# Kernel tuning notes

Hardware: AMD Instinct MI355X
Metric: run time of the kernel (lower is better)

The kernel has to match this reference:

```python
import jax, jax.numpy as jnp
import numpy as np

N, E, G = 50000, 800000, 64
IN, HID, T, EDGE_DIM, HLS = 32, 64, 2, 2, 32
# deg histogram: all nodes degree 16 -> avg_deg['log'] = log(16+1)
AVG_LOG = float(np.log(17.0))


def _pna(x, src, dst, eattr, We, be, Wpre, bpre, Wpost, bpost, Wlin, blin):
    """PNAConv with aggregators [mean,min,max,std], scalers [identity,amp,att],
    towers=T, pre_layers=1, post_layers=1, divide_input=False."""
    n, F = x.shape
    enc = eattr @ We + be                                   # [E, F] edge encoder
    # message: concat(x_i, x_j, edge) -> per-tower Linear(3F -> F)
    h = jnp.concatenate([x[dst], x[src], enc], axis=-1)     # [E, 3F] (same for all towers)
    m = jnp.einsum('ef,tfo->eto', h, Wpre) + bpre           # [E, T, F]
    ones = jnp.ones((m.shape[0],), m.dtype)
    cnt = jax.ops.segment_sum(ones, dst, num_segments=n)    # in-degree [N]
    d = jnp.maximum(cnt, 1.0)[:, None, None]
    s = jax.ops.segment_sum(m, dst, num_segments=n)
    mean = s / d
    msq = jax.ops.segment_sum(m * m, dst, num_segments=n) / d
    std = jnp.sqrt(jax.nn.relu(msq - mean * mean) + 1e-5)
    has = (cnt > 0)[:, None, None]
    mn = jnp.where(has, jax.ops.segment_min(m, dst, num_segments=n), 0.0)
    mx = jnp.where(has, jax.ops.segment_max(m, dst, num_segments=n), 0.0)
    agg = jnp.concatenate([mean, mn, mx, std], axis=-1)     # [N, T, 4F]
    logd = jnp.log(d + 1.0)
    scaled = jnp.concatenate([agg, agg * (logd / AVG_LOG), agg * (AVG_LOG / logd)], axis=-1)  # [N,T,12F]
    xt = jnp.broadcast_to(x[:, None, :], (n, Wpre.shape[0], F))
    out = jnp.concatenate([xt, scaled], axis=-1)            # [N, T, 13F]
    o = jnp.einsum('nti,tio->nto', out, Wpost) + bpost      # [N, T, F_out]
    return o.reshape(n, -1) @ Wlin + blin                   # [N, HID]


def setup_inputs():
    key = jax.random.key(0)
    ks = iter(jax.random.split(key, 48))
    def p(shape):
        return jax.random.normal(next(ks), shape, jnp.float32) * 0.05
    inp = {}
    inp['x'] = jax.random.normal(next(ks), (N, IN), jnp.float32)
    inp['edge_attr'] = jax.random.normal(next(ks), (E, EDGE_DIM), jnp.float32)
    inp['hls_attr'] = jax.random.normal(next(ks), (G, HLS), jnp.float32)
    inp['edge_index'] = jax.random.randint(next(ks), (2, E), 0, N)
    inp['batch'] = jnp.sort(jax.random.randint(next(ks), (N,), 0, G))
    Fo = HID // T
    for l, Fin in enumerate([IN, HID]):
        inp[f'We{l}'] = p((EDGE_DIM, Fin)); inp[f'be{l}'] = jnp.zeros((Fin,), jnp.float32)
        inp[f'Wpre{l}'] = p((T, 3 * Fin, Fin)); inp[f'bpre{l}'] = jnp.zeros((T, Fin), jnp.float32)
        inp[f'Wpost{l}'] = p((T, 13 * Fin, Fo)); inp[f'bpost{l}'] = jnp.zeros((T, Fo), jnp.float32)
        inp[f'Wlin{l}'] = p((HID, HID)); inp[f'blin{l}'] = jnp.zeros((HID,), jnp.float32)
    inp['W1'] = p((HID + HLS, 64)); inp['b1'] = jnp.zeros((64,), jnp.float32)
    inp['W2'] = p((64, 64)); inp['b2'] = jnp.zeros((64,), jnp.float32)
    inp['W3'] = p((64, 1)); inp['b3'] = jnp.zeros((1,), jnp.float32)
    return inp


def reference(x, edge_attr, hls_attr,
              We0, be0, Wpre0, bpre0, Wpost0, bpost0, Wlin0, blin0,
              We1, be1, Wpre1, bpre1, Wpost1, bpost1, Wlin1, blin1,
              W1, b1, W2, b2, W3, b3,
              edge_index, batch):
    src, dst = edge_index[0], edge_index[1]
    h = jax.nn.relu(_pna(x, src, dst, edge_attr, We0, be0, Wpre0, bpre0, Wpost0, bpost0, Wlin0, blin0))
    h = jax.nn.relu(_pna(h, src, dst, edge_attr, We1, be1, Wpre1, bpre1, Wpost1, bpost1, Wlin1, blin1))
    g = jax.ops.segment_sum(h, batch, num_segments=G)       # global_add_pool [G, HID]
    g = jnp.concatenate([g, hls_attr], axis=-1)
    g = jax.nn.relu(g @ W1 + b1)
    g = jax.nn.relu(g @ W2 + b2)
    return g @ W3 + b3                                      # [G, 1]
```

## Files before the change

kernel.cpp:

```cpp
#include <hip/hip_runtime.h>
#include <math.h>
#include <float.h>

#define NN 50000
#define EE 800000
#define CAP 64
#define CPAD 16

typedef unsigned short ushort_t;
typedef short short8 __attribute__((ext_vector_type(8)));
typedef float floatx4 __attribute__((ext_vector_type(4)));

__device__ __constant__ float kAVG_LOG = 2.8332133440562162f;

__device__ inline ushort_t f2bf(float v) {
    union { float f; unsigned u; } x; x.f = v;
    unsigned r = x.u + 0x7fffu + ((x.u >> 16) & 1u);
    return (ushort_t)(r >> 16);
}
__device__ inline float bf2f(ushort_t b) {
    union { unsigned u; float f; } x; x.u = ((unsigned)b) << 16; return x.f;
}
__device__ inline float bitsf(unsigned u) {
    union { unsigned u; float f; } x; x.u = u; return x.f;
}
__device__ inline void splitbf(float v, ushort_t& hi, ushort_t& lo) {
    hi = f2bf(v);
    lo = f2bf(v - bf2f(hi));
}

template <int F>
__device__ void prep_ab_dev(const float* __restrict__ We, const float* __restrict__ be,
                            const float* __restrict__ Wpre, const float* __restrict__ bpre,
                            float* __restrict__ U, float* __restrict__ Wab,
                            float* __restrict__ bias_ab) {
    const int TF = 2 * F;
    int tid = threadIdx.x;
    for (int idx = tid; idx < 2 * TF; idx += 256) {
        int c = idx / TF, f = idx % TF;
        int t = f / F, o = f % F;
        float s = 0.f;
        for (int g = 0; g < F; ++g)
            s += We[c * F + g] * Wpre[((size_t)t * 3 * F + 2 * F + g) * F + o];
        U[idx] = s;
    }
    for (int idx = tid; idx < F * 2 * TF; idx += 256) {
        int g = idx / (2 * TF), cc = idx % (2 * TF);
        int t, o, row;
        if (cc < TF) { t = cc / F; o = cc % F; row = g; }
        else { int c2 = cc - TF; t = c2 / F; o = c2 % F; row = F + g; }
        Wab[idx] = Wpre[((size_t)t * 3 * F + row) * F + o];
    }
    for (int cc = tid; cc < 2 * TF; cc += 256) {
        float v = 0.f;
        if (cc < TF) {
            int t = cc / F, o = cc % F;
            float s = 0.f;
            for (int g = 0; g < F; ++g)
                s += be[g] * Wpre[((size_t)t * 3 * F + 2 * F + g) * F + o];
            v = s + bpre[t * F + o];
        }
        bias_ab[cc] = v;
    }
}

template <int F>
__device__ void prep_zf_elem(int idx, const float* __restrict__ Wpost, const float* __restrict__ Wlin,
                             ushort_t* __restrict__ Bh, ushort_t* __restrict__ Bl) {
    const int KT = 9 * F;
    int jg = idx / KT, k = idx - jg * KT;
    int b = jg >> 6, j = jg & 63;
    float v = 0.f;
    if (k < F) {
        if (b == 0) {
#pragma unroll
            for (int t = 0; t < 2; ++t)
#pragma unroll
                for (int c = 0; c < 32; ++c)
                    v += Wpost[((size_t)t * 13 * F + k) * 32 + c] * Wlin[(t * 32 + c) * 64 + j];
        }
    } else {
        int r = k - F;
        int t = r / (4 * F), rr = r - t * 4 * F;
#pragma unroll
        for (int c = 0; c < 32; ++c)
            v += Wpost[((size_t)t * 13 * F + F + b * 4 * F + rr) * 32 + c] * Wlin[(t * 32 + c) * 64 + j];
    }
    ushort_t h_, l_;
    splitbf(v, h_, l_);
    Bh[(size_t)jg * KT + k] = h_;
    Bl[(size_t)jg * KT + k] = l_;
}

#define NZ0 216
#define NZ1 432
#define PREPB (NZ0 + NZ1 + 3)
#define INITB 6250

__global__ __launch_bounds__(256) void prep_init(
    const float* We0, const float* be0, const float* Wpre0, const float* bpre0,
    const float* Wpost0, const float* Wlin0, const float* bpost0, const float* blin0,
    const float* We1, const float* be1, const float* Wpre1, const float* bpre1,
    const float* Wpost1, const float* Wlin1, const float* bpost1, const float* blin1,
    float* U0, float* Wab0, float* bias_ab0, ushort_t* Bh0, ushort_t* Bl0, float* bias_zf0,
    float* U1, float* Wab1, float* bias_ab1, ushort_t* Bh1, ushort_t* Bl1, float* bias_zf1,
    int* cnt, float* pool, const float* __restrict__ x, ushort_t* __restrict__ xb) {
    int b = blockIdx.x;
    int tid = threadIdx.x;
    if (b >= PREPB) {
        int i = (b - PREPB) * 256 + tid;
        if (i < NN * 32) xb[i] = f2bf(x[i]);
        if (i < NN * CPAD) cnt[i] = 0;
        if (i < 64 * 64) pool[i] = 0.f;
        return;
    }
    if (b < NZ0) {
        prep_zf_elem<32>(b * 256 + tid, Wpost0, Wlin0, Bh0, Bl0);
    } else if (b < NZ0 + NZ1) {
        prep_zf_elem<64>((b - NZ0) * 256 + tid, Wpost1, Wlin1, Bh1, Bl1);
    } else if (b == NZ0 + NZ1) {
        prep_ab_dev<32>(We0, be0, Wpre0, bpre0, U0, Wab0, bias_ab0);
    } else if (b == NZ0 + NZ1 + 1) {
        prep_ab_dev<64>(We1, be1, Wpre1, bpre1, U1, Wab1, bias_ab1);
    } else {
        for (int j = tid; j < 64; j += 256) {
            float s0 = blin0[j], s1 = blin1[j];
#pragma unroll
            for (int t = 0; t < 2; ++t)
#pragma unroll
                for (int c = 0; c < 32; ++c) {
                    s0 += bpost0[t * 32 + c] * Wlin0[(t * 32 + c) * 64 + j];
                    s1 += bpost1[t * 32 + c] * Wlin1[(t * 32 + c) * 64 + j];
                }
            bias_zf0[j] = s0;
            bias_zf1[j] = s1;
        }
    }
}

__device__ void gemm_bias_block(const float* __restrict__ A, const float* __restrict__ B,
                                const float* __restrict__ bias, float* __restrict__ Ca,
                                ushort_t* __restrict__ Cb, int M, int K, int Ncols, int bstart,
                                int mb, int cb) {
    __shared__ float As[32][132];
    __shared__ float Bs[32][68];
    int m0 = mb * 128, c0 = cb * 64;
    int tid = threadIdx.x;
    int tx = tid & 15, ty = tid >> 4;
    int ms = tid >> 3, u = tid & 7;
    float acc[8][4] = {};
    for (int k0 = 0; k0 < K; k0 += 32) {
#pragma unroll
        for (int p = 0; p < 4; ++p) {
            int m = ms + 32 * p;
            int gm = m0 + m;
            float4 v = make_float4(0.f, 0.f, 0.f, 0.f);
            if (gm < M) v = *(const float4*)(A + (size_t)gm * K + k0 + u * 4);
            As[u * 4 + 0][m] = v.x; As[u * 4 + 1][m] = v.y;
            As[u * 4 + 2][m] = v.z; As[u * 4 + 3][m] = v.w;
        }
#pragma unroll
        for (int p = 0; p < 2; ++p) {
            int idx = tid + 256 * p;
            int kk = idx >> 4, q = idx & 15;
            *(float4*)&Bs[kk][q * 4] = *(const float4*)(B + (size_t)(k0 + kk) * Ncols + c0 + q * 4);
        }
        __syncthreads();
#pragma unroll 8
        for (int k = 0; k < 32; ++k) {
            float a0[8], b0[4];
            *(float4*)&a0[0] = *(const float4*)&As[k][ty * 8];
            *(float4*)&a0[4] = *(const float4*)&As[k][ty * 8 + 4];
            *(float4*)&b0[0] = *(const float4*)&Bs[k][tx * 4];
#pragma unroll
            for (int i = 0; i < 8; ++i)
#pragma unroll
                for (int j = 0; j < 4; ++j) acc[i][j] = fmaf(a0[i], b0[j], acc[i][j]);
        }
        __syncthreads();
    }
    float bj[4];
#pragma unroll
    for (int j = 0; j < 4; ++j) bj[j] = bias[c0 + tx * 4 + j];
    bool bside = (c0 >= bstart);
    int TFw = bstart;
#pragma unroll
    for (int i = 0; i < 8; ++i) {
        int gm = m0 + ty * 8 + i;
        if (gm >= M) continue;
        float v0 = acc[i][0] + bj[0], v1 = acc[i][1] + bj[1];
        float v2 = acc[i][2] + bj[2], v3 = acc[i][3] + bj[3];
        if (!bside) {
            *(float4*)(Ca + (size_t)gm * TFw + c0 + tx * 4) = make_float4(v0, v1, v2, v3);
        } else {
            ushort4 w;
            w.x = f2bf(v0); w.y = f2bf(v1); w.z = f2bf(v2); w.w = f2bf(v3);
            *(ushort4*)(Cb + (size_t)gm * TFw + (c0 - bstart) + tx * 4) = w;
        }
    }
}

__global__ __launch_bounds__(256) void gemm_bias(const float* __restrict__ A, const float* __restrict__ B,
                                                 const float* __restrict__ bias, float* __restrict__ Ca,
                                                 ushort_t* __restrict__ Cb, int M, int K, int Ncols, int bstart) {
    gemm_bias_block(A, B, bias, Ca, Cb, M, K, Ncols, bstart, blockIdx.x, blockIdx.y);
}

__global__ __launch_bounds__(256) void csr_gemm0(
    const int* __restrict__ ei, const float* __restrict__ ea,
    int* __restrict__ cnt, uint2* __restrict__ csr,
    const float* __restrict__ A, const float* __restrict__ B, const float* __restrict__ bias,
    float* __restrict__ Ca, ushort_t* __restrict__ Cb) {
    int bx = blockIdx.x;
    if (bx % 5 == 0) {
        int g = bx / 5;
        gemm_bias_block(A, B, bias, Ca, Cb, NN, 32, 128, 64, g % 391, g / 391);
    } else {
        int ce = bx - 1 - bx / 5;
        int e = ce * 256 + threadIdx.x;
        if (e >= EE) return;
        int s = ei[e];
        int d = ei[EE + e];
        float2 v = *(const float2*)(ea + 2 * e);
        int p = atomicAdd(&cnt[d * CPAD], 1);
        if (p < CAP) {
            uint2 w;
            w.x = (unsigned)s;
            w.y = ((unsigned)f2bf(v.y) << 16) | (unsigned)f2bf(v.x);
            csr[d * CAP + p] = w;
        }
    }
}

template <int F>
__global__ __launch_bounds__(256) void aggregate(const float* __restrict__ ABa, const ushort_t* __restrict__ ABb,
                                                 const int* __restrict__ cnt, const uint2* __restrict__ csr,
                                                 const float* __restrict__ U,
                                                 ushort_t* __restrict__ agg_b, float2* __restrict__ sc) {
    const int TF = 2 * F;
    const int FPL = TF / 64;
    int lane = threadIdx.x & 63;
    int n = blockIdx.x * 4 + (threadIdx.x >> 6);
    if (n >= NN) return;
    int f0 = FPL * lane;

    float base[FPL], u0[FPL], u1[FPL], sum[FPL], sq[FPL], mn[FPL], mx[FPL];
#pragma unroll
    for (int r = 0; r < FPL; ++r) {
        base[r] = ABa[(size_t)n * TF + f0 + r];
        u0[r] = U[f0 + r];
        u1[r] = U[TF + f0 + r];
        sum[r] = 0.f; sq[r] = 0.f; mn[r] = FLT_MAX; mx[r] = -FLT_MAX;
    }
    int deg = cnt[n * CPAD];
    int ec = deg < CAP ? deg : CAP;
    if (ec > 0) {
        int ebase = n * CAP;
        int myi = lane < ec ? lane : ec - 1;
        uint2 ent = csr[ebase + myi];
        int msrc = (int)ent.x;
        unsigned mea = ent.y;
        int e = 0;
        for (; e + 8 <= ec; e += 8) {
            int sb[8]; unsigned ep[8];
            unsigned wv[8];
#pragma unroll
            for (int i = 0; i < 8; ++i) {
                sb[i] = __shfl(msrc, e + i);
                ep[i] = (unsigned)__shfl((int)mea, e + i);
            }
#pragma unroll
            for (int i = 0; i < 8; ++i) {
                if constexpr (FPL == 2)
                    wv[i] = *(const unsigned*)(ABb + (size_t)sb[i] * TF + f0);
                else
                    wv[i] = ABb[(size_t)sb[i] * TF + f0];
            }
#pragma unroll
            for (int i = 0; i < 8; ++i) {
                float ex = bitsf(ep[i] << 16);
                float ey = bitsf(ep[i] & 0xffff0000u);
                float v[FPL];
                if constexpr (FPL == 2) {
                    v[0] = bitsf(wv[i] << 16);
                    v[1] = bitsf(wv[i] & 0xffff0000u);
                } else {
                    v[0] = bitsf(wv[i] << 16);
                }
#pragma unroll
                for (int r = 0; r < FPL; ++r) {
                    float q = fmaf(ex, u0[r], fmaf(ey, u1[r], v[r]));
                    sum[r] += q;
                    sq[r] = fmaf(q, q, sq[r]);
                    mn[r] = fminf(mn[r], q);
                    mx[r] = fmaxf(mx[r], q);
                }
            }
        }
        if (e < ec) {
            int sb[8]; unsigned ep[8];
            unsigned wv[8];
#pragma unroll
            for (int i = 0; i < 8; ++i) {
                sb[i] = __shfl(msrc, e + i);
                ep[i] = (unsigned)__shfl((int)mea, e + i);
            }
#pragma unroll
            for (int i = 0; i < 8; ++i) {
                if (e + i < ec) {
                    if constexpr (FPL == 2)
                        wv[i] = *(const unsigned*)(ABb + (size_t)sb[i] * TF + f0);
                    else
                        wv[i] = ABb[(size_t)sb[i] * TF + f0];
                }
            }
#pragma unroll
            for (int i = 0; i < 8; ++i) {
                if (e + i < ec) {
                    float ex = bitsf(ep[i] << 16);
                    float ey = bitsf(ep[i] & 0xffff0000u);
                    float v[FPL];
                    if constexpr (FPL == 2) {
                        v[0] = bitsf(wv[i] << 16);
                        v[1] = bitsf(wv[i] & 0xffff0000u);
                    } else {
                        v[0] = bitsf(wv[i] << 16);
                    }
#pragma unroll
                    for (int r = 0; r < FPL; ++r) {
                        float q = fmaf(ex, u0[r], fmaf(ey, u1[r], v[r]));
                        sum[r] += q;
                        sq[r] = fmaf(q, q, sq[r]);
                        mn[r] = fminf(mn[r], q);
                        mx[r] = fmaxf(mx[r], q);
                    }
                }
            }
        }
    }
    float d = (float)(deg > 1 ? deg : 1);
    float inv_d = 1.f / d;
    bool has = deg > 0;
#pragma unroll
    for (int r = 0; r < FPL; ++r) {
        float mean_q = sum[r] * inv_d;
        float var = sq[r] * inv_d - mean_q * mean_q;
        float stdv = sqrtf(fmaxf(var, 0.f) + 1e-5f);
        float mean = has ? base[r] + mean_q : 0.f;
        float vmn = has ? base[r] + mn[r] : 0.f;
        float vmx = has ? base[r] + mx[r] : 0.f;
        int f = f0 + r;
        int t = f / F, o = f - t * F;
        size_t rowb = (size_t)n * (4 * TF) + (size_t)t * (4 * F);
        agg_b[rowb + o] = f2bf(mean);
        agg_b[rowb + F + o] = f2bf(vmn);
        agg_b[rowb + 2 * F + o] = f2bf(vmx);
        agg_b[rowb + 3 * F + o] = f2bf(stdv);
    }
    if (lane == 0) {
        float logd = logf(d + 1.f);
        sc[n] = make_float2(logd / kAVG_LOG, kAVG_LOG / logd);
    }
}

template <int F, bool POOL>
__global__ __launch_bounds__(256, 2) void gemm_zf(
    const ushort_t* __restrict__ xs_b, const ushort_t* __restrict__ agg_b,
    const ushort_t* __restrict__ Bh, const ushort_t* __restrict__ Bl,
    const float* __restrict__ bias_zf, const float2* __restrict__ sc,
    float* __restrict__ H, ushort_t* __restrict__ H_b,
    const int* __restrict__ batch, float* __restrict__ pool) {
    const int KT = 9 * F;
    extern __shared__ char smem[];
    ushort_t* A_s  = (ushort_t*)smem;
    ushort_t* Bh_s = A_s + 128 * 40;
    ushort_t* Bl_s = Bh_s + 192 * 40;
    float* hbuf = (float*)smem;

    int m0 = blockIdx.x * 128;
    int tid = threadIdx.x;
    int lane = tid & 63;
    int wave = tid >> 6;
    int ln = lane & 15, quad = lane >> 4;

    floatx4 acc[8][3];
#pragma unroll
    for (int i = 0; i < 8; ++i)
#pragma unroll
        for (int j = 0; j < 3; ++j) acc[i][j] = (floatx4)(0.f);

    int arow = tid >> 2, asg = tid & 3;
    int bcol[3], bsg[3];
#pragma unroll
    for (int p = 0; p < 3; ++p) {
        int idx = tid + 256 * p;
        bcol[p] = idx >> 2;
        bsg[p] = idx & 3;
    }

    const short8 zero8 = {0, 0, 0, 0, 0, 0, 0, 0};
    short8 pa[2], pbh[3], pbl[3];
    {
        int c0 = asg * 8;
#pragma unroll
        for (int q = 0; q < 2; ++q) {
            int gm = m0 + arow + q * 64;
            pa[q] = zero8;
            if (gm < NN) pa[q] = *(const short8*)(xs_b + (size_t)gm * F + c0);
        }
#pragma unroll
        for (int p = 0; p < 3; ++p) {
            pbh[p] = *(const short8*)(Bh + (size_t)bcol[p] * KT + bsg[p] * 8);
            pbl[p] = *(const short8*)(Bl + (size_t)bcol[p] * KT + bsg[p] * 8);
        }
    }

    for (int k0 = 0; k0 < KT; k0 += 32) {
#pragma unroll
        for (int q = 0; q < 2; ++q)
            *(short8*)&A_s[(arow + q * 64) * 40 + asg * 8] = pa[q];
#pragma unroll
        for (int p = 0; p < 3; ++p) {
            *(short8*)&Bh_s[bcol[p] * 40 + bsg[p] * 8] = pbh[p];
            *(short8*)&Bl_s[bcol[p] * 40 + bsg[p] * 8] = pbl[p];
        }
        __syncthreads();
        short8 bh[3], bl[3];
#pragma unroll
        for (int b = 0; b < 3; ++b) {
            int col = b * 64 + wave * 16 + ln;
            bh[b] = *(short8*)&Bh_s[col * 40 + quad * 8];
            bl[b] = *(short8*)&Bl_s[col * 40 + quad * 8];
        }
        int kn = k0 + 32;
        if (kn < KT) {
            int c0 = kn + asg * 8;
#pragma unroll
            for (int q = 0; q < 2; ++q) {
                int gm = m0 + arow + q * 64;
                pa[q] = zero8;
                if (gm < NN) {
                    pa[q] = (c0 < F) ? *(const short8*)(xs_b + (size_t)gm * F + c0)
                                     : *(const short8*)(agg_b + (size_t)gm * 8 * F + (c0 - F));
                }
            }
#pragma unroll
            for (int p = 0; p < 3; ++p) {
                pbh[p] = *(const short8*)(Bh + (size_t)bcol[p] * KT + kn + bsg[p] * 8);
                pbl[p] = *(const short8*)(Bl + (size_t)bcol[p] * KT + kn + bsg[p] * 8);
            }
        }
#pragma unroll
        for (int rf = 0; rf < 8; ++rf) {
            short8 ah = *(short8*)&A_s[(rf * 16 + ln) * 40 + quad * 8];
#pragma unroll
            for (int b = 0; b < 3; ++b) {
                acc[rf][b] = __builtin_amdgcn_mfma_f32_16x16x32_bf16(ah, bh[b], acc[rf][b], 0, 0, 0);
                acc[rf][b] = __builtin_amdgcn_mfma_f32_16x16x32_bf16(ah, bl[b], acc[rf][b], 0, 0, 0);
            }
        }
        __syncthreads();
    }

    int ocol = wave * 16 + ln;
    float bcolv = bias_zf[ocol];

    if (POOL) __syncthreads();

#pragma unroll
    for (int rf = 0; rf < 8; ++rf) {
#pragma unroll
        for (int reg = 0; reg < 4; ++reg) {
            int r = rf * 16 + quad * 4 + reg;
            int gm = m0 + r;
            float2 s = make_float2(0.f, 0.f);
            if (gm < NN) s = sc[gm];
            float y = acc[rf][0][reg] + s.x * acc[rf][1][reg] + s.y * acc[rf][2][reg] + bcolv;
            y = fmaxf(y, 0.f);
            if (POOL) {
                hbuf[r * 68 + ocol] = (gm < NN) ? y : 0.f;
            } else if (gm < NN) {
                H[(size_t)gm * 64 + ocol] = y;
                H_b[(size_t)gm * 64 + ocol] = f2bf(y);
            }
        }
    }
    if (POOL) {
        __syncthreads();
        int col = tid & 63, grp = tid >> 6;
        float a = 0.f;
        int cur = -1;
        for (int i = 0; i < 32; ++i) {
            int r = grp * 32 + i;
            int gm = m0 + r;
            if (gm >= NN) break;
            int b = batch[gm];
            if (b != cur) {
                if (cur >= 0) atomicAdd(&pool[cur * 64 + col], a);
                cur = b; a = 0.f;
            }
            a += hbuf[r * 68 + col];
        }
        if (cur >= 0) atomicAdd(&pool[cur * 64 + col], a);
    }
}

__global__ __launch_bounds__(256) void head_kernel(const float* __restrict__ gpool, const float* __restrict__ hls,
                                                   const float* __restrict__ W1, const float* __restrict__ b1,
                                                   const float* __restrict__ W2, const float* __restrict__ b2,
                                                   const float* __restrict__ W3, const float* __restrict__ b3,
                                                   float* __restrict__ out) {
    __shared__ float gin[64][96];
    __shared__ float r1[64][64];
    __shared__ float r2[64][64];
    int tid = threadIdx.x;
    for (int idx = tid; idx < 64 * 96; idx += 256) {
        int g = idx / 96, j = idx % 96;
        gin[g][j] = (j < 64) ? gpool[g * 64 + j] : hls[g * 32 + (j - 64)];
    }
    __syncthreads();
    for (int idx = tid; idx < 64 * 64; idx += 256) {
        int g = idx / 64, j = idx % 64;
        float acc = b1[j];
        for (int k = 0; k < 96; ++k) acc = fmaf(gin[g][k], W1[k * 64 + j], acc);
        r1[g][j] = fmaxf(acc, 0.f);
    }
    __syncthreads();
    for (int idx = tid; idx < 64 * 64; idx += 256) {
        int g = idx / 64, j = idx % 64;
        float acc = b2[j];
        for (int k = 0; k < 64; ++k) acc = fmaf(r1[g][k], W2[k * 64 + j], acc);
        r2[g][j] = fmaxf(acc, 0.f);
    }
    __syncthreads();
    if (tid < 64) {
        float acc = b3[0];
        for (int k = 0; k < 64; ++k) acc = fmaf(r2[tid][k], W3[k], acc);
        out[tid] = acc;
    }
}

extern "C" void kernel_launch(void* const* d_in, const int* in_sizes, int n_in,
                              void* d_out, int out_size, void* d_ws, size_t ws_size,
                              hipStream_t stream) {
    (void)in_sizes; (void)n_in; (void)out_size; (void)ws_size;
    const float* x     = (const float*)d_in[0];
    const float* eattr = (const float*)d_in[1];
    const float* hls   = (const float*)d_in[2];
    const int*   eidx  = (const int*)d_in[3];
    const int*   batch = (const int*)d_in[4];
    const float* We[2]    = {(const float*)d_in[5],  (const float*)d_in[13]};
    const float* be[2]    = {(const float*)d_in[6],  (const float*)d_in[14]};
    const float* Wpre[2]  = {(const float*)d_in[7],  (const float*)d_in[15]};
    const float* bpre[2]  = {(const float*)d_in[8],  (const float*)d_in[16]};
    const float* Wpost[2] = {(const float*)d_in[9],  (const float*)d_in[17]};
    const float* bpost[2] = {(const float*)d_in[10], (const float*)d_in[18]};
    const float* Wlin[2]  = {(const float*)d_in[11], (const float*)d_in[19]};
    const float* blin[2]  = {(const float*)d_in[12], (const float*)d_in[20]};
    const float* W1 = (const float*)d_in[21]; const float* b1 = (const float*)d_in[22];
    const float* W2 = (const float*)d_in[23]; const float* b2 = (const float*)d_in[24];
    const float* W3 = (const float*)d_in[25]; const float* b3 = (const float*)d_in[26];
    float* out = (float*)d_out;

    char* ws = (char*)d_ws;
    size_t off = 0;
    auto carve = [&](size_t bytes) -> char* {
        char* p = ws + off;
        off = (off + bytes + 255) & ~(size_t)255;
        return p;
    };
    int*      cnt      = (int*)carve((size_t)NN * CPAD * 4);
    uint2*    csr      = (uint2*)carve((size_t)NN * CAP * 8);
    float*    ABa      = (float*)carve((size_t)NN * 128 * 4);
    ushort_t* ABb      = (ushort_t*)carve((size_t)NN * 128 * 2);
    ushort_t* agg_b    = (ushort_t*)carve((size_t)NN * 512 * 2);
    float2*   sc       = (float2*)carve((size_t)NN * 8);
    ushort_t* xs_b     = (ushort_t*)carve((size_t)NN * 32 * 2);
    float*    h1       = (float*)carve((size_t)NN * 64 * 4);
    ushort_t* h1_b     = (ushort_t*)carve((size_t)NN * 64 * 2);
    float*    U0       = (float*)carve(256 * 4);
    float*    U1       = (float*)carve(256 * 4);
    float*    Wab0     = (float*)carve(16384 * 4);
    float*    Wab1     = (float*)carve(16384 * 4);
    float*    bias_ab0 = (float*)carve(256 * 4);
    float*    bias_ab1 = (float*)carve(256 * 4);
    ushort_t* Bh0      = (ushort_t*)carve((size_t)192 * 288 * 2);
    ushort_t* Bl0      = (ushort_t*)carve((size_t)192 * 288 * 2);
    ushort_t* Bh1      = (ushort_t*)carve((size_t)192 * 576 * 2);
    ushort_t* Bl1      = (ushort_t*)carve((size_t)192 * 576 * 2);
    float*    bias_zf0 = (float*)carve(64 * 4);
    float*    bias_zf1 = (float*)carve(64 * 4);
    float*    pool     = (float*)carve(64 * 64 * 4);

    const int MB128 = (NN + 127) / 128;
    const int SMEM_ZF = (128 * 40 + 192 * 40 + 192 * 40) * 2;
    const int CSRB = (EE + 255) / 256;
    const int FUSEDB = CSRB + MB128 * 2;

    prep_init<<<PREPB + INITB, 256, 0, stream>>>(
        We[0], be[0], Wpre[0], bpre[0], Wpost[0], Wlin[0], bpost[0], blin[0],
        We[1], be[1], Wpre[1], bpre[1], Wpost[1], Wlin[1], bpost[1], blin[1],
        U0, Wab0, bias_ab0, Bh0, Bl0, bias_zf0,
        U1, Wab1, bias_ab1, Bh1, Bl1, bias_zf1,
        cnt, pool, x, xs_b);

    csr_gemm0<<<FUSEDB, 256, 0, stream>>>(eidx, eattr, cnt, csr, x, Wab0, bias_ab0, ABa, ABb);
    aggregate<32><<<(NN + 3) / 4, 256, 0, stream>>>(ABa, ABb, cnt, csr, U0, agg_b, sc);
    gemm_zf<32, false><<<MB128, 256, SMEM_ZF, stream>>>(xs_b, agg_b, Bh0, Bl0, bias_zf0, sc,
                                                        h1, h1_b, batch, pool);

    gemm_bias<<<dim3(MB128, 4), 256, 0, stream>>>(h1, Wab1, bias_ab1, ABa, ABb, NN, 64, 256, 128);
    aggregate<64><<<(NN + 3) / 4, 256, 0, stream>>>(ABa, ABb, cnt, csr, U1, agg_b, sc);
    gemm_zf<64, true><<<MB128, 256, SMEM_ZF, stream>>>(h1_b, agg_b, Bh1, Bl1, bias_zf1, sc,
                                                       nullptr, nullptr, batch, pool);

    head_kernel<<<1, 256, 0, stream>>>(pool, hls, W1, b1, W2, b2, W3, b3, out);
}
```

Before: 355.6 us.

## Build CSR via two-pass bucket partition with shared-memory atomics

Replaces direct global atomics on per-node counters with a two-stage build. First, edges are bucketed by destination block of 256 nodes using shared-memory histograms and one global atomic per bucket per block. Then each bucket is scattered into the per-node CSR with shared-memory atomics, and the GEMM blocks are interleaved in the same launch. This removes 800k contended global atomics and the padded counter array. It adds an extra kernel launch and a round trip of the partition buffer, which reuses agg_b, and edges are silently dropped if a bucket overflows its fixed capacity.

```diff
diff --git a/kernel.cpp b/kernel.cpp
--- a/kernel.cpp
+++ b/kernel.cpp
@@ -5,7 +5,10 @@
 #define NN 50000
 #define EE 800000
 #define CAP 64
-#define CPAD 16
+
+#define NB 196
+#define SPAN 256
+#define BCAP 4608
 
 typedef unsigned short ushort_t;
 typedef short short8 __attribute__((ext_vector_type(8)));
@@ -104,13 +107,13 @@
     const float* Wpost1, const float* Wlin1, const float* bpost1, const float* blin1,
     float* U0, float* Wab0, float* bias_ab0, ushort_t* Bh0, ushort_t* Bl0, float* bias_zf0,
     float* U1, float* Wab1, float* bias_ab1, ushort_t* Bh1, ushort_t* Bl1, float* bias_zf1,
-    int* cnt, float* pool, const float* __restrict__ x, ushort_t* __restrict__ xb) {
+    int* gcount, float* pool, const float* __restrict__ x, ushort_t* __restrict__ xb) {
     int b = blockIdx.x;
     int tid = threadIdx.x;
     if (b >= PREPB) {
         int i = (b - PREPB) * 256 + tid;
         if (i < NN * 32) xb[i] = f2bf(x[i]);
-        if (i < NN * CPAD) cnt[i] = 0;
+        if (i < NB) gcount[i] = 0;
         if (i < 64 * 64) pool[i] = 0.f;
         return;
     }
@@ -136,6 +139,70 @@
             bias_zf1[j] = s1;
         }
     }
+}
+
+__global__ __launch_bounds__(1024) void partition_edges(
+    const int* __restrict__ ei, const float* __restrict__ ea,
+    int* __restrict__ gcount, uint2* __restrict__ part) {
+    __shared__ int hist[NB];
+    __shared__ int lbase[NB];
+    int tid = threadIdx.x;
+    int e0 = blockIdx.x * 4096;
+    for (int i = tid; i < NB; i += 1024) hist[i] = 0;
+    __syncthreads();
+    int bq[4], rnk[4];
+    unsigned px[4], py[4];
+#pragma unroll
+    for (int q = 0; q < 4; ++q) {
+        int e = e0 + q * 1024 + tid;
+        bq[q] = -1;
+        if (e < EE) {
+            int s = ei[e];
+            int d = ei[EE + e];
+            float2 v = *(const float2*)(ea + 2 * e);
+            bq[q] = d >> 8;
+            px[q] = ((unsigned)(d & 255) << 16) | (unsigned)s;
+            py[q] = ((unsigned)f2bf(v.y) << 16) | (unsigned)f2bf(v.x);
+            rnk[q] = atomicAdd(&hist[bq[q]], 1);
+        }
+    }
+    __syncthreads();
+    for (int i = tid; i < NB; i += 1024)
+        lbase[i] = atomicAdd(&gcount[i], hist[i]);
+    __syncthreads();
+#pragma unroll
+    for (int q = 0; q < 4; ++q) {
+        if (bq[q] >= 0) {
+            int slot = lbase[bq[q]] + rnk[q];
+            if (slot < BCAP)
+                part[(size_t)bq[q] * BCAP + slot] = make_uint2(px[q], py[q]);
+        }
+    }
+}
+
+__device__ void csr_fill_block(int g, const int* __restrict__ gcount,
+                               const uint2* __restrict__ part,
+                               int* __restrict__ cnt, uint2* __restrict__ csr) {
+    __shared__ int lcnt[SPAN];
+    int tid = threadIdx.x;
+    lcnt[tid] = 0;
+    __syncthreads();
+    int total = gcount[g];
+    if (total > BCAP) total = BCAP;
+    size_t pbase = (size_t)g * BCAP;
+    for (int i = tid; i < total; i += 256) {
+        uint2 rec = part[pbase + i];
+        int rel = rec.x >> 16;
+        int src = rec.x & 0xffff;
+        int p = atomicAdd(&lcnt[rel], 1);
+        if (p < CAP) {
+            int node = (g << 8) + rel;
+            csr[(size_t)node * CAP + p] = make_uint2((unsigned)src, rec.y);
+        }
+    }
+    __syncthreads();
+    int node = (g << 8) + tid;
+    if (node < NN) cnt[node] = lcnt[tid];
 }
 
 __device__ void gemm_bias_block(const float* __restrict__ A, const float* __restrict__ B,
@@ -207,28 +274,16 @@
 }
 
 __global__ __launch_bounds__(256) void csr_gemm0(
-    const int* __restrict__ ei, const float* __restrict__ ea,
+    const int* __restrict__ gcount, const uint2* __restrict__ part,
     int* __restrict__ cnt, uint2* __restrict__ csr,
     const float* __restrict__ A, const float* __restrict__ B, const float* __restrict__ bias,
     float* __restrict__ Ca, ushort_t* __restrict__ Cb) {
     int bx = blockIdx.x;
     if (bx % 5 == 0) {
-        int g = bx / 5;
-        gemm_bias_block(A, B, bias, Ca, Cb, NN, 32, 128, 64, g % 391, g / 391);
+        csr_fill_block(bx / 5, gcount, part, cnt, csr);
     } else {
-        int ce = bx - 1 - bx / 5;
-        int e = ce * 256 + threadIdx.x;
-        if (e >= EE) return;
-        int s = ei[e];
-        int d = ei[EE + e];
-        float2 v = *(const float2*)(ea + 2 * e);
-        int p = atomicAdd(&cnt[d * CPAD], 1);
-        if (p < CAP) {
-            uint2 w;
-            w.x = (unsigned)s;
-            w.y = ((unsigned)f2bf(v.y) << 16) | (unsigned)f2bf(v.x);
-            csr[d * CAP + p] = w;
-        }
+        int idx = bx - 1 - bx / 5;
+        gemm_bias_block(A, B, bias, Ca, Cb, NN, 32, 128, 64, idx % 391, idx / 391);
     }
 }
 
@@ -252,7 +307,7 @@
         u1[r] = U[TF + f0 + r];
         sum[r] = 0.f; sq[r] = 0.f; mn[r] = FLT_MAX; mx[r] = -FLT_MAX;
     }
-    int deg = cnt[n * CPAD];
+    int deg = cnt[n];
     int ec = deg < CAP ? deg : CAP;
     if (ec > 0) {
         int ebase = n * CAP;
@@ -569,7 +624,7 @@
         off = (off + bytes + 255) & ~(size_t)255;
         return p;
     };
-    int*      cnt      = (int*)carve((size_t)NN * CPAD * 4);
+    int*      cnt      = (int*)carve((size_t)NN * 4);
     uint2*    csr      = (uint2*)carve((size_t)NN * CAP * 8);
     float*    ABa      = (float*)carve((size_t)NN * 128 * 4);
     ushort_t* ABb      = (ushort_t*)carve((size_t)NN * 128 * 2);
@@ -591,20 +646,23 @@
     float*    bias_zf0 = (float*)carve(64 * 4);
     float*    bias_zf1 = (float*)carve(64 * 4);
     float*    pool     = (float*)carve(64 * 64 * 4);
+    int*      gcount   = (int*)carve(NB * 4);
+    uint2*    part     = (uint2*)agg_b;
 
     const int MB128 = (NN + 127) / 128;
     const int SMEM_ZF = (128 * 40 + 192 * 40 + 192 * 40) * 2;
-    const int CSRB = (EE + 255) / 256;
-    const int FUSEDB = CSRB + MB128 * 2;
+    const int FUSEDB = NB + MB128 * 2;
 
     prep_init<<<PREPB + INITB, 256, 0, stream>>>(
         We[0], be[0], Wpre[0], bpre[0], Wpost[0], Wlin[0], bpost[0], blin[0],
         We[1], be[1], Wpre[1], bpre[1], Wpost[1], Wlin[1], bpost[1], blin[1],
         U0, Wab0, bias_ab0, Bh0, Bl0, bias_zf0,
         U1, Wab1, bias_ab1, Bh1, Bl1, bias_zf1,
-        cnt, pool, x, xs_b);
-
-    csr_gemm0<<<FUSEDB, 256, 0, stream>>>(eidx, eattr, cnt, csr, x, Wab0, bias_ab0, ABa, ABb);
+        gcount, pool, x, xs_b);
+
+    partition_edges<<<(EE + 4095) / 4096, 1024, 0, stream>>>(eidx, eattr, gcount, part);
+
+    csr_gemm0<<<FUSEDB, 256, 0, stream>>>(gcount, part, cnt, csr, x, Wab0, bias_ab0, ABa, ABb);
     aggregate<32><<<(NN + 3) / 4, 256, 0, stream>>>(ABa, ABb, cnt, csr, U0, agg_b, sc);
     gemm_zf<32, false><<<MB128, 256, SMEM_ZF, stream>>>(xs_b, agg_b, Bh0, Bl0, bias_zf0, sc,
                                                         h1, h1_b, batch, pool);
```

Result: faster. 330.1 us (-7.2%).
